# Kernel tuning notes

Measured on AMD Instinct MI355X. Metric: run time of the kernel, lower is better.

The kernel has to match this reference:

```python
import jax, jax.numpy as jnp
import numpy as np

LEAK = 0.2

def leaky(x):
    return jnp.where(x > 0, x, LEAK * x)

def relu(x):
    return jnp.maximum(x, 0)

def conv1d(x, w):
    # x [B,Cin,L], w [Cout,Cin,3], stride 1, padding 1
    return jax.lax.conv_general_dilated(x, w, (1,), [(1, 1)],
        dimension_numbers=('NCH', 'OIH', 'NCH'))

def conv2d(x, w, pad, dil=1, groups=1):
    return jax.lax.conv_general_dilated(x, w, (1, 1), [(pad, pad), (pad, pad)],
        rhs_dilation=(dil, dil), feature_group_count=groups,
        dimension_numbers=('NCHW', 'OIHW', 'NCHW'))

def bn2d(x, p, eps=1e-5):
    # p: [4,C] = gamma, beta, running_mean, running_var (eval-mode BN)
    g, b, m, v = p
    s = (1, -1, 1, 1)
    return (x - m.reshape(s)) * (g.reshape(s) / jnp.sqrt(v.reshape(s) + eps)) + b.reshape(s)

def layernorm(x, g, b, eps=1e-5):
    mu = x.mean(-1, keepdims=True)
    var = ((x - mu) ** 2).mean(-1, keepdims=True)
    return (x - mu) / jnp.sqrt(var + eps) * g + b

def l2n(x, axis, eps):
    n = jnp.sqrt((x * x).sum(axis, keepdims=True))
    return x / jnp.maximum(n, eps)


def setup_inputs() -> dict:
    key = jax.random.key(0)
    B, C, H, W = 4, 64, 48, 48
    D, Fn, T, V = 256, 8, 4, 16
    E = 16  # orthogonal prototype embed dim
    ks = iter(jax.random.split(key, 64))
    def rn(shape, s=0.05):
        return jax.random.normal(next(ks), shape, jnp.float32) * s
    def bnp(c):
        return jnp.stack([1.0 + rn((c,), 0.1), rn((c,), 0.1), rn((c,), 0.1), 1.0 + jnp.abs(rn((c,), 0.1))])
    return dict(
        basis_vector_bank=jax.random.normal(next(ks), (T, V, D), jnp.float32),
        task_f=jax.random.normal(next(ks), (B, C, 16, 16), jnp.float32),
        img_f=jax.random.normal(next(ks), (B, C, H, W), jnp.float32),
        protos=jax.random.normal(next(ks), (T, E), jnp.float32),
        tA_w1=rn((E // 4, 1, 3)), tA_w2=rn((E // 2, E // 4, 3)),
        iA_w=rn((E // 2, C, 3, 3)), iA_bn=bnp(E // 2),
        at_w1=rn((E, Fn // 2 * E)), at_b1=rn((Fn // 2 * E,)),
        at_ln_g=jnp.ones((Fn // 2 * E,)), at_ln_b=jnp.zeros((Fn // 2 * E,)),
        at_w2=rn((Fn // 2 * E, Fn * E)), at_b2=rn((Fn * E,)),
        bv_t1=rn((D // 4, 1, 3)), bv_t2=rn((D // 2, D // 4, 3)),
        bv_ic1=rn((D // 4, C, 3, 3)), bv_bn1=bnp(D // 4),
        bv_ic2=rn((D // 2, D // 4, 3, 3)), bv_bn2=bnp(D // 2),
        bv_w1=rn((D, D // 4)), bv_b1=rn((D // 4,)),
        bv_ln_g=jnp.ones((D // 4,)), bv_ln_b=jnp.zeros((D // 4,)),
        bv_w2=rn((D // 4, D)), bv_b2=rn((D,)),
        m1_w1=rn((D, D // 4)), m1_b1=rn((D // 4,)),
        m1_ln_g=jnp.ones((D // 4,)), m1_ln_b=jnp.zeros((D // 4,)),
        m1_w2=rn((D // 4, C * C)), m1_b2=rn((C * C,)),
        m3_w1=rn((D, D // 4)), m3_b1=rn((D // 4,)),
        m3_ln_g=jnp.ones((D // 4,)), m3_ln_b=jnp.zeros((D // 4,)),
        m3_w2=rn((D // 4, 9 * C * C)), m3_b2=rn((9 * C * C,)),
        blr_bn=bnp(C),
        zc_w=rn((C, C, 1, 1), 0.01), zc_b=rn((C,), 0.01),
    )


def _forward(basis_vector_bank, task_f, img_f, protos, tA_w1, tA_w2, iA_w, iA_bn,
             at_w1, at_b1, at_ln_g, at_ln_b, at_w2, at_b2,
             bv_t1, bv_t2, bv_ic1, bv_bn1, bv_ic2, bv_bn2,
             bv_w1, bv_b1, bv_ln_g, bv_ln_b, bv_w2, bv_b2,
             m1_w1, m1_b1, m1_ln_g, m1_ln_b, m1_w2, m1_b2,
             m3_w1, m3_b1, m3_ln_g, m3_ln_b, m3_w2, m3_b2,
             blr_bn, zc_w, zc_b):
    T, V, D = basis_vector_bank.shape
    B, C, H, W = img_f.shape
    E = protos.shape[1]
    Fn = at_w2.shape[1] // E
    tau = 0.5

    # --- A2SI routing features ---
    xt = task_f.reshape(B, 1, -1)
    t1 = conv1d(leaky(conv1d(xt, tA_w1)), tA_w2).mean(-1)          # [B,E/2]
    i1 = leaky(bn2d(conv2d(img_f, iA_w, 1), iA_bn)).mean((2, 3))   # [B,E/2]
    f1 = jnp.concatenate([t1, i1], axis=1)                         # [B,E]
    h = relu(layernorm(f1 @ at_w1 + at_b1, at_ln_g, at_ln_b))
    tif = (h @ at_w2 + at_b2).reshape(B, E, Fn)                    # [B,E,F]
    logits = jnp.einsum('te,bef->bft', l2n(protos, -1, 1e-8), l2n(tif, 1, 1e-8))  # [B,F,T]

    # hard gumbel-softmax (straight-through), fixed noise key for determinism
    u = jax.random.uniform(jax.random.key(42), logits.shape, jnp.float32, 1e-10, 1.0)
    g = -jnp.log(-jnp.log(u))
    y = jax.nn.softmax((logits + g) / tau, axis=-1)
    idx = jnp.argmax(y, axis=-1)                                   # [B,F]
    y_hard = jax.nn.one_hot(idx, T, dtype=y.dtype)
    set_type = y_hard + y - jax.lax.stop_gradient(y)

    bank_flat = basis_vector_bank.reshape(T, V * D)
    sbvb = jnp.einsum('bft,tk->bfk', set_type, bank_flat).reshape(B, Fn, V, D)

    # --- BasisV_filter: filter feature ---
    xt2 = task_f.reshape(B, C, -1)
    rms = jnp.sqrt((xt2 ** 2).mean((1, 2), keepdims=True))
    xt2 = (xt2 / (rms + 1e-8)).reshape(B, 1, -1)
    te = conv1d(leaky(conv1d(xt2, bv_t1)), bv_t2).mean(-1)         # [B,D/2]
    ie = leaky(bn2d(conv2d(img_f, bv_ic1, 1), bv_bn1))
    ie = leaky(bn2d(conv2d(ie, bv_ic2, 1), bv_bn2)).mean((2, 3))   # [B,D/2]
    ff = jnp.concatenate([te, ie], axis=1)                         # [B,D]
    ff = relu(layernorm(ff @ bv_w1 + bv_b1, bv_ln_g, bv_ln_b)) @ bv_w2 + bv_b2

    # --- per-(batch,type) group gather/top-k/scatter, vectorized ---
    # group bank = bank of first filter with that type (hard one-hot -> type's bank)
    occ = idx[:, None, :] == jnp.arange(T)[None, :, None]          # [B,T,F]
    first = jnp.argmax(occ, axis=-1)                               # [B,T]
    Bg = jnp.take_along_axis(sbvb, first[:, :, None, None], axis=1)  # [B,T,V,D]
    # all rows of Q within a group are identical (filter_f expanded over F),
    # so S.max(0) == cosine(ff[b], Bg[b,t])
    scores = jnp.einsum('bd,btvd->btv', l2n(ff, -1, 1e-12), l2n(Bg, -1, 1e-12))
    order = jnp.argsort(-scores, axis=-1)                          # [B,T,V] topk order
    lt = jnp.tril(jnp.ones((Fn, Fn), bool), -1)                    # j < i
    rank = ((idx[:, :, None] == idx[:, None, :]) & lt).sum(-1)     # position in group
    bidx = jnp.arange(B)[:, None]
    sel = order[bidx, idx, rank]                                   # [B,F]
    bvf = Bg[bidx, idx, sel]                                       # [B,F,D]

    # --- per-filter dynamic convolutions ---
    w1 = relu(layernorm(bvf @ m1_w1 + m1_b1, m1_ln_g, m1_ln_b)) @ m1_w2 + m1_b2
    w1 = w1.reshape(B, Fn, C, C)                                   # [B,F,out,in]
    w3 = relu(layernorm(bvf @ m3_w1 + m3_b1, m3_ln_g, m3_ln_b)) @ m3_w2 + m3_b2
    w3 = w3.reshape(B * Fn, C, C, 3, 3)

    dp0 = jnp.einsum('bfoc,bchw->bfohw', w1, img_f)                # 1x1 branch
    xin = jnp.broadcast_to(img_f[:, None], (B, Fn, C, H, W)).reshape(1, B * Fn * C, H, W)
    ker = w3.reshape(B * Fn * C, C, 3, 3)
    dpd = [conv2d(xin, ker, d, dil=d, groups=B * Fn).reshape(B, Fn, C, H, W)
           for d in (1, 2, 3)]                                     # same-padded dilated 3x3
    t_ = idx[:, :, None, None, None]
    dp = jnp.where(t_ == 0, dp0, jnp.where(t_ == 1, dpd[0],
         jnp.where(t_ == 2, dpd[1], dpd[2])))                      # [B,F,C,H,W]

    x = leaky(bn2d(dp.reshape(B * Fn, C, H, W), blr_bn)).reshape(B, Fn, C, H, W).mean(1)
    a = conv2d(x, zc_w, 0) + zc_b.reshape(1, -1, 1, 1)
    return a + img_f


@jax.jit
def reference(basis_vector_bank, task_f, img_f, protos, tA_w1, tA_w2, iA_w, iA_bn,
              at_w1, at_b1, at_ln_g, at_ln_b, at_w2, at_b2,
              bv_t1, bv_t2, bv_ic1, bv_bn1, bv_ic2, bv_bn2,
              bv_w1, bv_b1, bv_ln_g, bv_ln_b, bv_w2, bv_b2,
              m1_w1, m1_b1, m1_ln_g, m1_ln_b, m1_w2, m1_b2,
              m3_w1, m3_b1, m3_ln_g, m3_ln_b, m3_w2, m3_b2,
              blr_bn, zc_w, zc_b):
    return _forward(basis_vector_bank, task_f, img_f, protos, tA_w1, tA_w2, iA_w, iA_bn,
                    at_w1, at_b1, at_ln_g, at_ln_b, at_w2, at_b2,
                    bv_t1, bv_t2, bv_ic1, bv_bn1, bv_ic2, bv_bn2,
                    bv_w1, bv_b1, bv_ln_g, bv_ln_b, bv_w2, bv_b2,
                    m1_w1, m1_b1, m1_ln_g, m1_ln_b, m1_w2, m1_b2,
                    m3_w1, m3_b1, m3_ln_g, m3_ln_b, m3_w2, m3_b2,
                    blr_bn, zc_w, zc_b)
```

## Files before the change

### kernel.cpp

```cpp
#include <hip/hip_runtime.h>
#include <math.h>

#define LEAKC 0.2f

#define NB 4
#define NC 64
#define LLEN 16384
#define HW 2304
#define PP 54
#define PHW 2916
#define SLABP 72
#define CP 72
#define IE1C 50

typedef __attribute__((ext_vector_type(8))) short short8;
typedef __attribute__((ext_vector_type(4))) float floatx4;

__device__ __forceinline__ float leaky(float x){ return x > 0.f ? x : LEAKC*x; }

__device__ __forceinline__ float wave_sum64(float v){
  for(int off=32;off;off>>=1) v += __shfl_xor(v,off);
  return v;
}

__device__ __forceinline__ unsigned short f2bf(float x){
  unsigned u=__float_as_uint(x);
  unsigned r=u+0x7FFFu+((u>>16)&1u);
  return (unsigned short)(r>>16);
}

__device__ __forceinline__ void threefry2x32(unsigned k0, unsigned k1, unsigned& x0, unsigned& x1){
  unsigned ks0=k0, ks1=k1, ks2=k0^k1^0x1BD11BDAu;
  x0+=ks0; x1+=ks1;
  const int rot0[4]={13,15,26,6};
  const int rot1[4]={17,29,16,24};
#define TF_APPLY(rr) {for(int r=0;r<4;r++){x0+=x1; x1=(x1<<rr[r])|(x1>>(32-rr[r])); x1^=x0;}}
  TF_APPLY(rot0); x0+=ks1; x1+=ks2+1u;
  TF_APPLY(rot1); x0+=ks2; x1+=ks0+2u;
  TF_APPLY(rot0); x0+=ks0; x1+=ks1+3u;
  TF_APPLY(rot1); x0+=ks1; x1+=ks2+4u;
  TF_APPLY(rot0); x0+=ks2; x1+=ks0+5u;
#undef TF_APPLY
}

__device__ __forceinline__ float jax_uniform128(int i){
  unsigned x0=0u, x1=(unsigned)i;
  threefry2x32(0u,42u,x0,x1);
  unsigned bits = x0 ^ x1;
  unsigned fb=(bits>>9)|0x3f800000u;
  float f=__uint_as_float(fb)-1.0f;
  float u=f*(1.0f-1e-10f)+1e-10f;
  return fmaxf(1e-10f,u);
}

__global__ __launch_bounds__(256) void k_pre(const float* __restrict__ task_f,
                      const float* __restrict__ w1A, const float* __restrict__ w1B,
                      float* __restrict__ totApart, float* __restrict__ a0A, float* __restrict__ aLA,
                      float* __restrict__ totBpart, float* __restrict__ a0B, float* __restrict__ aLB,
                      float* __restrict__ rmspart,
                      const float* __restrict__ img,
                      const float* __restrict__ w1, const float* __restrict__ w2,
                      const float* __restrict__ wa,
                      unsigned short* __restrict__ imgTP,
                      unsigned short* __restrict__ W1T, unsigned short* __restrict__ W2T,
                      unsigned short* __restrict__ WAT,
                      const float* __restrict__ mw1, const float* __restrict__ mw3,
                      const float* __restrict__ bvw1p, const float* __restrict__ bvw2p,
                      const float* __restrict__ bvt2p, const float* __restrict__ atw2p,
                      const float* __restrict__ bankp, float* __restrict__ warm){
  if(blockIdx.x<256){
    int b=blockIdx.x>>6, seg=blockIdx.x&63;
    const float* x=task_f+b*LLEN;
    float tA[4]={0,0,0,0};
    float tB[64];
#pragma unroll
    for(int c=0;c<64;c++) tB[c]=0.f;
    float sq=0.f;
    int l=seg*256+threadIdx.x;
    {
      float xm=(l>0)?x[l-1]:0.f;
      float xc=x[l];
      float xp=(l<LLEN-1)?x[l+1]:0.f;
      sq=xc*xc;
#pragma unroll
      for(int c=0;c<4;c++){
        float a=leaky(w1A[c*3+0]*xm + w1A[c*3+1]*xc + w1A[c*3+2]*xp);
        tA[c]=a;
        if(l==0) a0A[b*4+c]=a;
        if(l==LLEN-1) aLA[b*4+c]=a;
      }
#pragma unroll
      for(int c=0;c<64;c++){
        float a=leaky(w1B[c*3+0]*xm + w1B[c*3+1]*xc + w1B[c*3+2]*xp);
        tB[c]=a;
        if(l==0) a0B[b*64+c]=a;
        if(l==LLEN-1) aLB[b*64+c]=a;
      }
    }
    sq=wave_sum64(sq);
#pragma unroll
    for(int c=0;c<4;c++) tA[c]=wave_sum64(tA[c]);
#pragma unroll
    for(int c=0;c<64;c++){
      float v=tB[c];
      for(int off=32;off;off>>=1) v+=__shfl_down(v,off);
      tB[c]=v;
    }
    __shared__ float redB[4][64];
    __shared__ float redA[4][4];
    __shared__ float redQ[4];
    int wave=threadIdx.x>>6, lane=threadIdx.x&63;
    if(lane==0){
#pragma unroll
      for(int c=0;c<64;c++) redB[wave][c]=tB[c];
#pragma unroll
      for(int c=0;c<4;c++) redA[wave][c]=tA[c];
      redQ[wave]=sq;
    }
    __syncthreads();
    if(threadIdx.x<64){
      float s=redB[0][threadIdx.x]+redB[1][threadIdx.x]+redB[2][threadIdx.x]+redB[3][threadIdx.x];
      totBpart[(size_t)(b*64+seg)*64+threadIdx.x]=s;
    } else if(threadIdx.x<68){
      int c=threadIdx.x-64;
      totApart[(b*64+seg)*4+c]=redA[0][c]+redA[1][c]+redA[2][c]+redA[3][c];
    } else if(threadIdx.x==68){
      rmspart[b*64+seg]=redQ[0]+redQ[1]+redQ[2]+redQ[3];
    }
  } else if(blockIdx.x<400){
    int blk=blockIdx.x-256;
    int b=blk/36, t=blk%36;
    int p0=t*64;
    __shared__ float tile[64][65];
    int pp=threadIdx.x&63, c4=threadIdx.x>>6;
    for(int r=0;r<16;r++){
      int c=c4*16+r;
      tile[c][pp]=img[(b*64+c)*HW + p0+pp];
    }
    __syncthreads();
    int pxl=threadIdx.x>>2, cg=(threadIdx.x&3)*16;
    unsigned out[8];
#pragma unroll
    for(int q=0;q<8;q++){
      unsigned lo=f2bf(tile[cg+2*q][pxl]);
      unsigned hi=f2bf(tile[cg+2*q+1][pxl]);
      out[q]=lo|(hi<<16);
    }
    int px=p0+pxl;
    int h=px/48, w=px-h*48;
    int poff=(h+3)*PP+(w+3);
    unsigned* dst=(unsigned*)(imgTP + ((size_t)(b*PHW+poff))*64 + cg);
#pragma unroll
    for(int q=0;q<8;q++) dst[q]=out[q];
  } else if(blockIdx.x<868){
    int n=(blockIdx.x-400)*256+threadIdx.x;
    if(n<9*64*64){
      int tap=n>>12, oc=(n>>6)&63, c=n&63;
      W1T[n]=f2bf(w1[oc*576+c*9+tap]);
    } else if(n<9*64*64+9*128*64){
      int m=n-9*64*64;
      int tap=m/8192, r=m-tap*8192, oc=r>>6, c=r&63;
      W2T[m]=f2bf(w2[oc*576+c*9+tap]);
    } else {
      int q=n-9*64*64-9*128*64;
      if(q<9*16*64){
        int tap=q>>10, r=q&1023, o=r>>6, c=r&63;
        WAT[q]=(o<8)?f2bf(wa[o*576+c*9+tap]):(unsigned short)0;
      }
    }
  } else if(blockIdx.x<884){
    int t=(blockIdx.x-868)*256+threadIdx.x;
    float a=0.f;
    for(int i=t;i*16<16384;i+=4096) a+=mw1[i*16];
    for(int i=t;i*16<16384;i+=4096) a+=mw3[i*16];
    for(int i=t;i*16<16384;i+=4096) a+=bvw1p[i*16];
    for(int i=t;i*16<16384;i+=4096) a+=bvw2p[i*16];
    for(int i=t;i*16<24576;i+=4096) a+=bvt2p[i*16];
    for(int i=t;i*16<8192;i+=4096) a+=atw2p[i*16];
    for(int i=t;i*16<16384;i+=4096) a+=bankp[i*16];
    warm[t&1023]=a;
  } else {
    int id=(blockIdx.x-884)*256+threadIdx.x;
    uint4 z=make_uint4(0,0,0,0);
    for(int cch=id;cch<19584;cch+=4096){
      int ck=cch&7, pxid=cch>>3;
      int b=pxid/612, p=pxid-b*612;
      int h,w;
      if(p<324){ int r=p/54; w=p-r*54; h=(r<3)?r:(r+48); }
      else { int q=p-324; int r2=q/6; int cc=q-r2*6; h=3+r2; w=(cc<3)?cc:(cc+48); }
      *(uint4*)(imgTP + ((size_t)(b*PHW + h*PP + w))*64 + ck*8)=z;
    }
  }
}

__global__ __launch_bounds__(512) void k_conv12(const unsigned short* __restrict__ imgTP,
                        const unsigned short* __restrict__ W1T,
                        const unsigned short* __restrict__ W2T,
                        const unsigned short* __restrict__ WAT,
                        const float* __restrict__ bn1, const float* __restrict__ bn2,
                        const float* __restrict__ bnA,
                        float* __restrict__ iepart, float* __restrict__ i1part){
  int tid=threadIdx.x;
  int lane=tid&63, wv=tid>>6;
  int n0=lane&15, kg=lane>>4;
  if(blockIdx.x<96){
    int blk=blockIdx.x;
    int b=blk/24, hp=blk-b*24;
    int h0=hp*2;
    __shared__ unsigned short slab[6*54*SLABP];
    __shared__ unsigned short ie1[4*IE1C*CP];
    {
      const unsigned short* ibase=imgTP+((size_t)b*PHW+(size_t)(h0+1)*PP)*64;
      for(int e=tid;e<6*54*8;e+=512){
        int rr=e/(54*8), rem=e-rr*54*8, w=rem>>3, ck=rem&7;
        uint4 v=*(const uint4*)(ibase+((size_t)(rr*PP+w))*64+ck*8);
        *(uint4*)(slab+(rr*54+w)*SLABP+ck*8)=v;
      }
      if(tid<64){
        int br=tid>>4, cq=(tid>>3)&1, ck=tid&7;
        *(uint4*)(ie1+((size_t)(br*IE1C+(cq?49:0)))*CP+ck*8)=make_uint4(0,0,0,0);
      }
    }
    __syncthreads();
    {
      int mt=wv&3, rh=wv>>2;
      floatx4 acc[2][3];
#pragma unroll
      for(int rr=0;rr<2;rr++)
#pragma unroll
        for(int nt=0;nt<3;nt++) acc[rr][nt]=(floatx4){0.f,0.f,0.f,0.f};
#pragma unroll
      for(int ti=0;ti<3;ti++){
#pragma unroll
        for(int tj=0;tj<3;tj++){
          int tap=ti*3+tj;
          const unsigned short* Ab=W1T+(size_t)tap*4096;
#pragma unroll
          for(int c0=0;c0<64;c0+=32){
            short8 a=*(const short8*)(Ab+((mt*16+n0)*64+c0+kg*8));
#pragma unroll
            for(int rr=0;rr<2;rr++){
              int sr=rh*2+rr+ti;
#pragma unroll
              for(int nt=0;nt<3;nt++){
                int sc=nt*16+n0+tj+2;
                short8 bv=*(const short8*)(slab+(sr*54+sc)*SLABP+c0+kg*8);
                acc[rr][nt]=__builtin_amdgcn_mfma_f32_16x16x32_bf16(a,bv,acc[rr][nt],0,0,0);
              }
            }
          }
        }
      }
      int obase=mt*16+kg*4;
      float scale[4],m_[4],be_[4];
#pragma unroll
      for(int reg=0;reg<4;reg++){
        int o=obase+reg;
        scale[reg]=bn1[o]/sqrtf(bn1[192+o]+1e-5f);
        m_[reg]=bn1[128+o]; be_[reg]=bn1[64+o];
      }
#pragma unroll
      for(int rr=0;rr<2;rr++){
        int br=rh*2+rr;
        bool rv=((unsigned)(h0-1+br))<48u;
#pragma unroll
        for(int nt=0;nt<3;nt++){
          float v0=rv?leaky((acc[rr][nt][0]-m_[0])*scale[0]+be_[0]):0.f;
          float v1=rv?leaky((acc[rr][nt][1]-m_[1])*scale[1]+be_[1]):0.f;
          float v2=rv?leaky((acc[rr][nt][2]-m_[2])*scale[2]+be_[2]):0.f;
          float v3=rv?leaky((acc[rr][nt][3]-m_[3])*scale[3]+be_[3]):0.f;
          unsigned w0=f2bf(v0)|((unsigned)f2bf(v1)<<16);
          unsigned w1=f2bf(v2)|((unsigned)f2bf(v3)<<16);
          uint2 pk={w0,w1};
          *(uint2*)(ie1+((size_t)(br*IE1C+(nt*16+1+n0)))*CP+obase)=pk;
        }
      }
    }
    __syncthreads();
    {
      int mt2=wv;
      floatx4 acc[6];
#pragma unroll
      for(int i=0;i<6;i++) acc[i]=(floatx4){0.f,0.f,0.f,0.f};
#pragma unroll
      for(int ti=0;ti<3;ti++){
#pragma unroll
        for(int tj=0;tj<3;tj++){
          int tap=ti*3+tj;
          const unsigned short* Ab=W2T+(size_t)tap*8192;
#pragma unroll
          for(int c0=0;c0<64;c0+=32){
            short8 a=*(const short8*)(Ab+((mt2*16+n0)*64+c0+kg*8));
#pragma unroll
            for(int rr=0;rr<2;rr++){
              int sr=rr+ti;
#pragma unroll
              for(int wc=0;wc<3;wc++){
                int q=wc*16+n0+tj;
                short8 bv=*(const short8*)(ie1+((size_t)(sr*IE1C+q))*CP+c0+kg*8);
                acc[rr*3+wc]=__builtin_amdgcn_mfma_f32_16x16x32_bf16(a,bv,acc[rr*3+wc],0,0,0);
              }
            }
          }
        }
      }
      int obase=mt2*16+kg*4;
#pragma unroll
      for(int reg=0;reg<4;reg++){
        int o=obase+reg;
        float scale=bn2[o]/sqrtf(bn2[384+o]+1e-5f);
        float m_=bn2[256+o], be_=bn2[128+o];
        float part=0;
#pragma unroll
        for(int i=0;i<6;i++) part+=leaky((acc[i][reg]-m_)*scale+be_);
        for(int off=1;off<16;off<<=1) part+=__shfl_xor(part,off);
        if(n0==0) iepart[(b*24+hp)*128+o]=part*(1.f/2304.f);
      }
    }
  } else {
    int blk2=blockIdx.x-96;
    int b=blk2/3, hg=blk2-b*3;
    int hp=hg*8+wv;
    int h0=hp*2;
    const unsigned short* ib=imgTP+(size_t)b*PHW*64;
    floatx4 acc[6];
#pragma unroll
    for(int i=0;i<6;i++) acc[i]=(floatx4){0.f,0.f,0.f,0.f};
#pragma unroll
    for(int ti=0;ti<3;ti++){
#pragma unroll
      for(int tj=0;tj<3;tj++){
        int tap=ti*3+tj;
        const unsigned short* Ab=WAT+(size_t)tap*1024;
#pragma unroll
        for(int c0=0;c0<64;c0+=32){
          short8 a=*(const short8*)(Ab+(n0*64+c0+kg*8));
#pragma unroll
          for(int rr=0;rr<2;rr++){
            int r=h0+rr+ti-1+3;
#pragma unroll
            for(int wc=0;wc<3;wc++){
              int w=wc*16+n0+tj-1+3;
              short8 bv=*(const short8*)(ib+((size_t)(r*PP+w)*64+c0+kg*8));
              acc[rr*3+wc]=__builtin_amdgcn_mfma_f32_16x16x32_bf16(a,bv,acc[rr*3+wc],0,0,0);
            }
          }
        }
      }
    }
    int obase=kg*4;
#pragma unroll
    for(int reg=0;reg<4;reg++){
      int o=obase+reg;
      float part=0;
      if(o<8){
        float scale=bnA[o]/sqrtf(bnA[24+o]+1e-5f);
        float m_=bnA[16+o], be_=bnA[8+o];
#pragma unroll
        for(int i=0;i<6;i++) part+=leaky((acc[i][reg]-m_)*scale+be_);
      }
      for(int off=1;off<16;off<<=1) part+=__shfl_xor(part,off);
      if(n0==0 && o<8) i1part[(b*24+hp)*8+o]=part*(1.f/2304.f);
    }
  }
}

__global__ __launch_bounds__(512,1) void k_mid(
    const float* __restrict__ totApart, const float* __restrict__ a0A, const float* __restrict__ aLA,
    const float* __restrict__ totBpart, const float* __restrict__ a0B, const float* __restrict__ aLB,
    const float* __restrict__ rmspart,
    const float* __restrict__ tA_w2, const float* __restrict__ bv_t2,
    const float* __restrict__ i1part, const float* __restrict__ iepart,
    const float* __restrict__ at_w1, const float* __restrict__ at_b1,
    const float* __restrict__ at_ln_g, const float* __restrict__ at_ln_b,
    const float* __restrict__ at_w2, const float* __restrict__ at_b2,
    const float* __restrict__ protos,
    const float* __restrict__ bv_w1, const float* __restrict__ bv_b1,
    const float* __restrict__ bv_ln_g, const float* __restrict__ bv_ln_b,
    const float* __restrict__ bv_w2, const float* __restrict__ bv_b2,
    const float* __restrict__ bank,
    const float* __restrict__ m1_w1, const float* __restrict__ m1_b1,
    const float* __restrict__ m1_g,  const float* __restrict__ m1_bb,
    const float* __restrict__ m3_w1, const float* __restrict__ m3_b1,
    const float* __restrict__ m3_g,  const float* __restrict__ m3_bb,
    int* __restrict__ idxo, float* __restrict__ hid1, float* __restrict__ hid3){
  int b=blockIdx.x;
  int tid=threadIdx.x;
  int lane=tid&63, wv=tid>>6;
  const float invL=1.0f/16384.0f;
  __shared__ float sT[64], s0[64], sL[64];
  __shared__ float totA_s[4];
  __shared__ float rms_s;
  __shared__ float part[512];
  __shared__ float te_s[128], t1_s[8];
  __shared__ float f1[16], h[64], tif[128], tifn[128], tden[8], pden[4], pn[64], z[32];
  __shared__ int sidx[8], sfirst[4], srank[8], rows[8];
  __shared__ float fbuf[256], hh[64], ffn_s[256], finv_s;
  __shared__ float scores[64];
  __shared__ int order[64];
  __shared__ float bvf[2048];

  if(tid<64){
    float s=0;
#pragma unroll 8
    for(int seg=0;seg<64;seg++) s+=totBpart[(size_t)(b*64+seg)*64+tid];
    sT[tid]=s;
  } else if(tid<128){
    int t=tid-64;
    s0[t]=a0B[b*64+t]; sL[t]=aLB[b*64+t];
  } else if(tid<192){
    float v=rmspart[b*64+(tid-128)];
    v=wave_sum64(v);
    if(tid==128) rms_s=v;
  } else if(tid<256){
    int c=tid-192;
    if(c<4){
      float s=0;
#pragma unroll 8
      for(int seg=0;seg<64;seg++) s+=totApart[(b*64+seg)*4+c];
      totA_s[c]=s;
    }
  }
  __syncthreads();
  float scB=1.0f/(sqrtf(rms_s*invL)+1e-8f);
  if(tid<256){
    int c2=tid&127, h2=tid>>7;
    const float* wr=bv_t2+c2*192;
    float s=0;
    for(int c1=h2*32;c1<h2*32+32;c1+=8){
      float4 q[6];
      const float4* r4=(const float4*)(wr+c1*3);
#pragma unroll
      for(int u=0;u<6;u++) q[u]=r4[u];
      const float* qq=(const float*)q;
#pragma unroll
      for(int u=0;u<8;u++){
        int c=c1+u;
        float T=sT[c], A0=s0[c], AL=sL[c];
        s += qq[u*3+0]*(T-AL) + qq[u*3+1]*T + qq[u*3+2]*(T-A0);
      }
    }
    part[tid]=s;
  } else if(tid>=384 && tid<392){
    int c2=tid-384;
    float s=0;
    for(int c1=0;c1<4;c1++){
      float T=totA_s[c1], A0=a0A[b*4+c1], AL=aLA[b*4+c1];
      const float* w=&tA_w2[(c2*4+c1)*3];
      s += w[0]*(T-AL) + w[1]*T + w[2]*(T-A0);
    }
    t1_s[c2]=s*invL;
  }
  __syncthreads();
  if(tid<128) te_s[tid]=(part[tid]+part[tid+128])*invL*scB;
  __syncthreads();

  if(tid<8) f1[tid]=t1_s[tid];
  else if(tid<16){
    int f=tid-8;
    float s=0;
#pragma unroll
    for(int g=0;g<24;g++) s+=i1part[(b*24+g)*8+f];
    f1[tid]=s;
  }
  __syncthreads();
  if(tid<64){
    float s=at_b1[lane];
#pragma unroll
    for(int i=0;i<16;i++) s+=f1[i]*at_w1[i*64+lane];
    float mu=wave_sum64(s)*(1.f/64.f);
    float d=s-mu;
    float var=wave_sum64(d*d)*(1.f/64.f);
    h[lane]=fmaxf(d*(1.0f/sqrtf(var+1e-5f))*at_ln_g[lane]+at_ln_b[lane],0.f);
  }
  __syncthreads();
  if(tid<256){
    int n=tid&127, h2=tid>>7;
    float a0=0,a1=0;
    for(int k=h2*32;k<h2*32+32;k+=2){
      a0+=h[k]*at_w2[k*128+n];
      a1+=h[k+1]*at_w2[(k+1)*128+n];
    }
    part[tid]=a0+a1;
  }
  __syncthreads();
  if(tid<128) tif[tid]=at_b2[tid]+part[tid]+part[tid+128];
  __syncthreads();
  if(tid<8){
    int f=tid;
    float ss=0; for(int e=0;e<16;e++){float v=tif[e*8+f]; ss+=v*v;}
    tden[f]=fmaxf(sqrtf(ss),1e-8f);
  } else if(tid<12){
    int t=tid-8;
    float ss=0; for(int e=0;e<16;e++){float v=protos[t*16+e]; ss+=v*v;}
    pden[t]=fmaxf(sqrtf(ss),1e-8f);
  }
  __syncthreads();
  if(tid<128) tifn[tid]=tif[tid]/tden[tid&7];
  if(tid<64) pn[tid]=protos[tid]/pden[tid>>4];
  __syncthreads();
  if(tid<32){
    int f=tid>>2, t=tid&3;
    float ss=0;
#pragma unroll
    for(int e=0;e<16;e++) ss+=pn[t*16+e]*tifn[e*8+f];
    float u=jax_uniform128(b*32+f*4+t);
    float g=-logf(-logf(u));
    z[tid]=ss+g;
  }
  __syncthreads();
  if(tid<8){
    float best=z[tid*4]; int bi=0;
    for(int t=1;t<4;t++){ float v=z[tid*4+t]; if(v>best){best=v;bi=t;} }
    sidx[tid]=bi;
  }
  __syncthreads();
  if(tid<4){
    int t=tid;
    int fi=0;
    for(int f=7;f>=0;f--) if(sidx[f]==t) fi=f;
    sfirst[t]=fi;
  } else if(tid<12){
    int f=tid-4;
    int c=0; for(int f2=0;f2<f;f2++) if(sidx[f2]==sidx[f]) c++;
    srank[f]=c;
  }
  __syncthreads();

  if(tid<128) fbuf[tid]=te_s[tid];
  else if(tid<256){
    int c=tid-128;
    float s=0;
#pragma unroll 8
    for(int g=0;g<24;g++) s+=iepart[(b*24+g)*128+c];
    fbuf[tid]=s;
  }
  __syncthreads();
  if(tid<256){
    int l64=tid&63, q=tid>>6;
    float a0=0,a1=0,a2=0,a3=0;
    for(int k=q*64;k<q*64+64;k+=4){
      a0+=fbuf[k]  *bv_w1[k*64+l64];
      a1+=fbuf[k+1]*bv_w1[(k+1)*64+l64];
      a2+=fbuf[k+2]*bv_w1[(k+2)*64+l64];
      a3+=fbuf[k+3]*bv_w1[(k+3)*64+l64];
    }
    part[tid]=((a0+a1)+(a2+a3));
  }
  __syncthreads();
  if(tid<64){
    float s=bv_b1[lane]+part[lane]+part[64+lane]+part[128+lane]+part[192+lane];
    float mu=wave_sum64(s)*(1.f/64.f);
    float d=s-mu;
    float var=wave_sum64(d*d)*(1.f/64.f);
    hh[lane]=fmaxf(d*(1.0f/sqrtf(var+1e-5f))*bv_ln_g[lane]+bv_ln_b[lane],0.f);
  }
  __syncthreads();
  {
    int n=tid&255, h2=tid>>8;
    float a0=0,a1=0;
    for(int k=h2*32;k<h2*32+32;k+=2){
      a0+=hh[k]*bv_w2[k*256+n];
      a1+=hh[k+1]*bv_w2[(k+1)*256+n];
    }
    part[tid]=a0+a1;
  }
  __syncthreads();
  if(tid<256) ffn_s[tid]=bv_b2[tid]+part[tid]+part[tid+256];
  __syncthreads();
  if(tid<64){
    float sq=0;
#pragma unroll
    for(int u=0;u<4;u++){ float v=ffn_s[u*64+lane]; sq+=v*v; }
    sq=wave_sum64(sq);
    if(lane==0) finv_s=1.0f/fmaxf(sqrtf(sq),1e-12f);
  }
  __syncthreads();
  if(tid<256) ffn_s[tid]*=finv_s;
  __syncthreads();

  if(tid<128){
    int it=tid&63, h2=tid>>6;
    int t=it>>4, v=it&15;
    int tt=sidx[sfirst[t]];
    const float4* row=(const float4*)(bank+(tt*16+v)*256);
    float sa=0,na=0;
    for(int d4=h2*32;d4<h2*32+32;d4++){
      float4 r=row[d4];
      const float* fp=&ffn_s[d4*4];
      sa+=fp[0]*r.x+fp[1]*r.y+fp[2]*r.z+fp[3]*r.w;
      na+=r.x*r.x+r.y*r.y+r.z*r.z+r.w*r.w;
    }
    part[tid]=sa;
    part[256+tid]=na;
  }
  __syncthreads();
  if(tid<64) scores[tid]=(part[tid]+part[tid+64])/fmaxf(sqrtf(part[256+tid]+part[320+tid]),1e-12f);
  __syncthreads();
  if(tid<4){
    const float* sc=&scores[tid*16];
    unsigned used=0;
    for(int pk=0;pk<16;pk++){
      int best=-1; float bv=-1e30f;
      for(int v2=0;v2<16;v2++){
        if(used&(1u<<v2)) continue;
        float vv=sc[v2];
        if(best<0||vv>bv){bv=vv;best=v2;}
      }
      used|=1u<<best;
      order[tid*16+pk]=best;
    }
  }
  __syncthreads();
  if(tid<8){
    int t=sidx[tid];
    int v=order[t*16+srank[tid]];
    rows[tid]=t*16+v;
    idxo[b*8+tid]=t;
  }
  __syncthreads();

  for(int ii=tid;ii<2048;ii+=512){
    int r=ii>>8, d=ii&255;
    bvf[ii]=bank[rows[r]*256+d];
  }
  __syncthreads();
  {
    int r=wv;
    const float* bp=&bvf[r*256];
    float a0=0,a1=0,a2=0,a3=0;
    float c0=0,c1=0,c2=0,c3=0;
    for(int d=0;d<256;d+=4){
      float b0=bp[d],b1=bp[d+1],b2=bp[d+2],b3=bp[d+3];
      a0+=b0*m1_w1[d*64+lane];
      a1+=b1*m1_w1[(d+1)*64+lane];
      a2+=b2*m1_w1[(d+2)*64+lane];
      a3+=b3*m1_w1[(d+3)*64+lane];
      c0+=b0*m3_w1[d*64+lane];
      c1+=b1*m3_w1[(d+1)*64+lane];
      c2+=b2*m3_w1[(d+2)*64+lane];
      c3+=b3*m3_w1[(d+3)*64+lane];
    }
    float s1=m1_b1[lane]+((a0+a1)+(a2+a3));
    float s3=m3_b1[lane]+((c0+c1)+(c2+c3));
    float mu=wave_sum64(s1)*(1.f/64.f);
    float dd=s1-mu;
    float var=wave_sum64(dd*dd)*(1.f/64.f);
    hid1[(b*8+r)*64+lane]=fmaxf(dd*(1.0f/sqrtf(var+1e-5f))*m1_g[lane]+m1_bb[lane],0.f);
    mu=wave_sum64(s3)*(1.f/64.f);
    dd=s3-mu;
    var=wave_sum64(dd*dd)*(1.f/64.f);
    hid3[(b*8+r)*64+lane]=fmaxf(dd*(1.0f/sqrtf(var+1e-5f))*m3_g[lane]+m3_bb[lane],0.f);
  }
}

__global__ __launch_bounds__(256) void k_heads(const float* __restrict__ hid1, const float* __restrict__ hid3,
                        const float* __restrict__ w2a, const float* __restrict__ b2a,
                        const float* __restrict__ w2b, const float* __restrict__ b2b,
                        unsigned short* __restrict__ A1, unsigned short* __restrict__ A3){
  __shared__ float hl[2048];
  if(blockIdx.x<16){
    int n=blockIdx.x*256+threadIdx.x;
    for(int i=threadIdx.x;i<2048;i+=256) hl[i]=hid1[i];
    __syncthreads();
    float wcol[64];
#pragma unroll
    for(int k=0;k<64;k++) wcol[k]=w2a[k*4096+n];
    float bb=b2a[n];
    for(int bf=0;bf<32;bf++){
      float s=bb;
#pragma unroll
      for(int k=0;k<64;k++) s+=hl[bf*64+k]*wcol[k];
      A1[bf*4096+n]=f2bf(s);
    }
  } else {
    int n=(blockIdx.x-16)*256+threadIdx.x;
    for(int i=threadIdx.x;i<2048;i+=256) hl[i]=hid3[i];
    __syncthreads();
    float wcol[64];
#pragma unroll
    for(int k=0;k<64;k++) wcol[k]=w2b[(size_t)k*36864+n];
    float bb=b2b[n];
    int o=n/576, rem=n-o*576;
    int c=rem/9, tap=rem-c*9;
    size_t base=((size_t)tap*64+o)*64+c;
    for(int bf=0;bf<32;bf++){
      float s=bb;
#pragma unroll
      for(int k=0;k<64;k++) s+=hl[bf*64+k]*wcol[k];
      A3[(size_t)bf*9*4096+base]=f2bf(s);
    }
  }
}

__global__ __launch_bounds__(512) void k_dynF(const unsigned short* __restrict__ imgTP,
                       const unsigned short* __restrict__ A1, const unsigned short* __restrict__ A3,
                       const int* __restrict__ idx, const float* __restrict__ bn,
                       const float* __restrict__ zc_w, const float* __restrict__ zc_b,
                       const float* __restrict__ img, float* __restrict__ out){
  int blk=blockIdx.x;
  int b=blk/48, r0=blk-b*48;
  int tid=threadIdx.x;
  int lane=tid&63, w8=tid>>6;
  int mt=w8&3, fh=w8>>2;
  int n0=lane&15, kg=lane>>4;
  __shared__ unsigned short slab[7*54*SLABP];
  __shared__ float xl[64*50];
  __shared__ float zl[4096];
  for(int i=tid;i<4096;i+=512) zl[i]=zc_w[i];
  for(int i=tid;i<3200;i+=512) xl[i]=0.f;
  {
    const unsigned short* ibase=imgTP+((size_t)b*PHW+(size_t)r0*PP)*64;
    for(int e=tid;e<7*54*8;e+=512){
      int rr=e/(54*8), rem=e-rr*54*8, w=rem>>3, ck=rem&7;
      uint4 v=*(const uint4*)(ibase + ((size_t)(rr*PP+w))*64 + ck*8);
      *(uint4*)(slab + (rr*54+w)*SLABP + ck*8)=v;
    }
  }
  __syncthreads();
  int obase=mt*16+kg*4;
  float scale[4],m_[4],be_[4];
#pragma unroll
  for(int reg=0;reg<4;reg++){
    int o=obase+reg;
    scale[reg]=bn[o]/sqrtf(bn[192+o]+1e-5f);
    m_[reg]=bn[128+o]; be_[reg]=bn[64+o];
  }
  float xsum[3][4];
#pragma unroll
  for(int wc=0;wc<3;wc++)
#pragma unroll
    for(int reg=0;reg<4;reg++) xsum[wc][reg]=0.f;
  for(int f=fh*4;f<fh*4+4;f++){
    int bf=b*8+f;
    int tt=idx[bf];
    floatx4 acc[3];
#pragma unroll
    for(int i=0;i<3;i++) acc[i]=(floatx4){0.f,0.f,0.f,0.f};
    if(tt==0){
      const unsigned short* Ab=A1+(size_t)bf*4096;
#pragma unroll
      for(int c0=0;c0<64;c0+=32){
        short8 a=*(const short8*)(Ab+((mt*16+n0)*64+c0+kg*8));
#pragma unroll
        for(int wc=0;wc<3;wc++){
          short8 bv=*(const short8*)(slab + (3*54 + wc*16+n0+3)*SLABP + c0+kg*8);
          acc[wc]=__builtin_amdgcn_mfma_f32_16x16x32_bf16(a,bv,acc[wc],0,0,0);
        }
      }
    } else {
      int d=tt;
      const unsigned short* A3b=A3+(size_t)bf*9*4096;
#pragma unroll
      for(int ti=0;ti<3;ti++){
        int lr=d*(ti-1)+3;
#pragma unroll
        for(int tj=0;tj<3;tj++){
          int tap=ti*3+tj;
          int dw=d*(tj-1)+3;
          const unsigned short* Ab=A3b+(size_t)tap*4096;
#pragma unroll
          for(int c0=0;c0<64;c0+=32){
            short8 a=*(const short8*)(Ab+((mt*16+n0)*64+c0+kg*8));
#pragma unroll
            for(int wc=0;wc<3;wc++){
              short8 bv=*(const short8*)(slab + (lr*54 + wc*16+n0+dw)*SLABP + c0+kg*8);
              acc[wc]=__builtin_amdgcn_mfma_f32_16x16x32_bf16(a,bv,acc[wc],0,0,0);
            }
          }
        }
      }
    }
#pragma unroll
    for(int wc=0;wc<3;wc++)
#pragma unroll
      for(int reg=0;reg<4;reg++)
        xsum[wc][reg]+=leaky((acc[wc][reg]-m_[reg])*scale[reg]+be_[reg]);
  }
#pragma unroll
  for(int wc=0;wc<3;wc++)
#pragma unroll
    for(int reg=0;reg<4;reg++)
      atomicAdd(&xl[(obase+reg)*50 + wc*16+n0], xsum[wc][reg]*0.125f);
  __syncthreads();
  size_t base=(size_t)b*64*HW + r0*48;
  for(int e=tid;e<3072;e+=512){
    int o=e/48, px=e-o*48;
    float s=zc_b[o];
#pragma unroll
    for(int c=0;c<64;c++) s+=zl[o*64+c]*xl[c*50+px];
    size_t a=base+(size_t)o*HW+px;
    out[a]=s+img[a];
  }
}

extern "C" void kernel_launch(void* const* d_in, const int* in_sizes, int n_in,
                              void* d_out, int out_size, void* d_ws, size_t ws_size,
                              hipStream_t stream){
  const float* bank   =(const float*)d_in[0];
  const float* task_f =(const float*)d_in[1];
  const float* img_f  =(const float*)d_in[2];
  const float* protos =(const float*)d_in[3];
  const float* tA_w1  =(const float*)d_in[4];
  const float* tA_w2  =(const float*)d_in[5];
  const float* iA_w   =(const float*)d_in[6];
  const float* iA_bn  =(const float*)d_in[7];
  const float* at_w1  =(const float*)d_in[8];
  const float* at_b1  =(const float*)d_in[9];
  const float* at_ln_g=(const float*)d_in[10];
  const float* at_ln_b=(const float*)d_in[11];
  const float* at_w2  =(const float*)d_in[12];
  const float* at_b2  =(const float*)d_in[13];
  const float* bv_t1  =(const float*)d_in[14];
  const float* bv_t2  =(const float*)d_in[15];
  const float* bv_ic1 =(const float*)d_in[16];
  const float* bv_bn1 =(const float*)d_in[17];
  const float* bv_ic2 =(const float*)d_in[18];
  const float* bv_bn2 =(const float*)d_in[19];
  const float* bv_w1  =(const float*)d_in[20];
  const float* bv_b1  =(const float*)d_in[21];
  const float* bv_ln_g=(const float*)d_in[22];
  const float* bv_ln_b=(const float*)d_in[23];
  const float* bv_w2  =(const float*)d_in[24];
  const float* bv_b2  =(const float*)d_in[25];
  const float* m1_w1  =(const float*)d_in[26];
  const float* m1_b1  =(const float*)d_in[27];
  const float* m1_ln_g=(const float*)d_in[28];
  const float* m1_ln_b=(const float*)d_in[29];
  const float* m1_w2  =(const float*)d_in[30];
  const float* m1_b2  =(const float*)d_in[31];
  const float* m3_w1  =(const float*)d_in[32];
  const float* m3_b1  =(const float*)d_in[33];
  const float* m3_ln_g=(const float*)d_in[34];
  const float* m3_ln_b=(const float*)d_in[35];
  const float* m3_w2  =(const float*)d_in[36];
  const float* m3_b2  =(const float*)d_in[37];
  const float* blr_bn =(const float*)d_in[38];
  const float* zc_w   =(const float*)d_in[39];
  const float* zc_b   =(const float*)d_in[40];

  float* ws=(float*)d_ws;
  float* totApart=ws+0;
  float* a0A  =ws+1024;
  float* aLA  =ws+1040;
  float* totBpart=ws+1056;
  float* a0B  =ws+17440;
  float* aLB  =ws+17696;
  float* rmspart=ws+17952;
  float* i1part =ws+18208;
  float* iepart =ws+18976;
  int*   idxp   =(int*)(ws+31264);
  float* hid1=ws+31296;
  float* hid3=ws+33344;
  unsigned short* A1p  =(unsigned short*)(ws+35392);
  unsigned short* A3p  =(unsigned short*)(ws+100928);
  unsigned short* imgTP=(unsigned short*)(ws+690752);
  unsigned short* W1Tp =(unsigned short*)(ws+1064000);
  unsigned short* W2Tp =(unsigned short*)(ws+1082432);
  unsigned short* WATp =(unsigned short*)(ws+1119296);
  float* warm =ws+1123904;

  k_pre<<<900,256,0,stream>>>(task_f, tA_w1, bv_t1,
                              totApart, a0A, aLA, totBpart, a0B, aLB, rmspart,
                              img_f, bv_ic1, bv_ic2, iA_w, imgTP, W1Tp, W2Tp, WATp,
                              m1_w1, m3_w1, bv_w1, bv_w2, bv_t2, at_w2, bank, warm);
  k_conv12<<<108,512,0,stream>>>(imgTP, W1Tp, W2Tp, WATp, bv_bn1, bv_bn2, iA_bn,
                                 iepart, i1part);
  k_mid<<<4,512,0,stream>>>(totApart,a0A,aLA,totBpart,a0B,aLB, rmspart, tA_w2, bv_t2,
                            i1part, iepart,
                            at_w1, at_b1, at_ln_g, at_ln_b, at_w2, at_b2, protos,
                            bv_w1, bv_b1, bv_ln_g, bv_ln_b, bv_w2, bv_b2, bank,
                            m1_w1, m1_b1, m1_ln_g, m1_ln_b,
                            m3_w1, m3_b1, m3_ln_g, m3_ln_b,
                            idxp, hid1, hid3);
  k_heads<<<160,256,0,stream>>>(hid1, hid3, m1_w2, m1_b2, m3_w2, m3_b2, A1p, A3p);
  k_dynF<<<192,512,0,stream>>>(imgTP, A1p, A3p, idxp, blr_bn, zc_w, zc_b, img_f, (float*)d_out);

  (void)in_sizes; (void)n_in; (void)out_size; (void)ws_size;
}
```

Baseline: 267.2 us.

## Expand cache prefetch warmup, parallelize k_mid reduction, hoist loads above barriers

The k_pre warm-up blocks grow from 16 to 64 and now also touch the large head weights (m1_w2, m3_w2) and zc_w at one line per 64 bytes, to pull them into L2 ahead of k_heads and k_dynF. k_mid spreads the totBpart reduction over all 512 threads with a shared-memory second stage, and its idle threads prefetch the weights it reads later. k_heads and k_dynF issue weight, idx and BN-parameter loads before the shared-memory fill and barrier so that latency overlaps. The cost is more global traffic and blocks in k_pre, plus an extra barrier in k_mid.

```diff
diff --git a/kernel.cpp b/kernel.cpp
--- a/kernel.cpp
+++ b/kernel.cpp
@@ -67,7 +67,10 @@
                       const float* __restrict__ mw1, const float* __restrict__ mw3,
                       const float* __restrict__ bvw1p, const float* __restrict__ bvw2p,
                       const float* __restrict__ bvt2p, const float* __restrict__ atw2p,
-                      const float* __restrict__ bankp, float* __restrict__ warm){
+                      const float* __restrict__ bankp,
+                      const float* __restrict__ m1w2p, const float* __restrict__ m3w2p,
+                      const float* __restrict__ zcwp,
+                      float* __restrict__ warm){
   if(blockIdx.x<256){
     int b=blockIdx.x>>6, seg=blockIdx.x&63;
     const float* x=task_f+b*LLEN;
@@ -168,19 +171,22 @@
         WAT[q]=(o<8)?f2bf(wa[o*576+c*9+tap]):(unsigned short)0;
       }
     }
-  } else if(blockIdx.x<884){
+  } else if(blockIdx.x<932){
     int t=(blockIdx.x-868)*256+threadIdx.x;
     float a=0.f;
-    for(int i=t;i*16<16384;i+=4096) a+=mw1[i*16];
-    for(int i=t;i*16<16384;i+=4096) a+=mw3[i*16];
-    for(int i=t;i*16<16384;i+=4096) a+=bvw1p[i*16];
-    for(int i=t;i*16<16384;i+=4096) a+=bvw2p[i*16];
-    for(int i=t;i*16<24576;i+=4096) a+=bvt2p[i*16];
-    for(int i=t;i*16<8192;i+=4096) a+=atw2p[i*16];
-    for(int i=t;i*16<16384;i+=4096) a+=bankp[i*16];
+    for(int i=t;i*16<16384;i+=16384) a+=mw1[i*16];
+    for(int i=t;i*16<16384;i+=16384) a+=mw3[i*16];
+    for(int i=t;i*16<16384;i+=16384) a+=bvw1p[i*16];
+    for(int i=t;i*16<16384;i+=16384) a+=bvw2p[i*16];
+    for(int i=t;i*16<24576;i+=16384) a+=bvt2p[i*16];
+    for(int i=t;i*16<8192;i+=16384) a+=atw2p[i*16];
+    for(int i=t;i*16<16384;i+=16384) a+=bankp[i*16];
+    for(int i=t;i*16<262144;i+=16384) a+=m1w2p[i*16];
+    for(int i=t;i*16<2359296;i+=16384) a+=m3w2p[i*16];
+    for(int i=t;i*16<4096;i+=16384) a+=zcwp[i*16];
     warm[t&1023]=a;
   } else {
-    int id=(blockIdx.x-884)*256+threadIdx.x;
+    int id=(blockIdx.x-932)*256+threadIdx.x;
     uint4 z=make_uint4(0,0,0,0);
     for(int cch=id;cch<19584;cch+=4096){
       int ck=cch&7, pxid=cch>>3;
@@ -389,6 +395,7 @@
   int lane=tid&63, wv=tid>>6;
   const float invL=1.0f/16384.0f;
   __shared__ float sT[64], s0[64], sL[64];
+  __shared__ float red8[64][9];
   __shared__ float totA_s[4];
   __shared__ float rms_s;
   __shared__ float part[512];
@@ -400,26 +407,46 @@
   __shared__ int order[64];
   __shared__ float bvf[2048];
 
-  if(tid<64){
-    float s=0;
-#pragma unroll 8
-    for(int seg=0;seg<64;seg++) s+=totBpart[(size_t)(b*64+seg)*64+tid];
-    sT[tid]=s;
-  } else if(tid<128){
+  {
+    int c8=tid>>3, g8=tid&7;
+    float s8=0;
+#pragma unroll
+    for(int seg=g8*8;seg<g8*8+8;seg++) s8+=totBpart[(size_t)(b*64+seg)*64+c8];
+    red8[c8][g8]=s8;
+  }
+  if(tid>=64 && tid<128){
     int t=tid-64;
     s0[t]=a0B[b*64+t]; sL[t]=aLB[b*64+t];
-  } else if(tid<192){
+  } else if(tid>=128 && tid<192){
     float v=rmspart[b*64+(tid-128)];
     v=wave_sum64(v);
     if(tid==128) rms_s=v;
-  } else if(tid<256){
+  } else if(tid>=192 && tid<196){
     int c=tid-192;
-    if(c<4){
-      float s=0;
+    float s=0;
 #pragma unroll 8
-      for(int seg=0;seg<64;seg++) s+=totApart[(b*64+seg)*4+c];
-      totA_s[c]=s;
-    }
+    for(int seg=0;seg<64;seg++) s+=totApart[(b*64+seg)*4+c];
+    totA_s[c]=s;
+  } else if(tid>=256){
+    int t=tid-256;
+    float ax=0.f,ay=0.f,az=0.f,aw=0.f;
+    const float4* p;
+    p=(const float4*)bv_t2;  for(int i=t;i<6144;i+=256){float4 v=p[i]; ax+=v.x;ay+=v.y;az+=v.z;aw+=v.w;}
+    p=(const float4*)at_w2;  for(int i=t;i<2048;i+=256){float4 v=p[i]; ax+=v.x;ay+=v.y;az+=v.z;aw+=v.w;}
+    p=(const float4*)bv_w1;  for(int i=t;i<4096;i+=256){float4 v=p[i]; ax+=v.x;ay+=v.y;az+=v.z;aw+=v.w;}
+    p=(const float4*)bv_w2;  for(int i=t;i<4096;i+=256){float4 v=p[i]; ax+=v.x;ay+=v.y;az+=v.z;aw+=v.w;}
+    p=(const float4*)m1_w1;  for(int i=t;i<4096;i+=256){float4 v=p[i]; ax+=v.x;ay+=v.y;az+=v.z;aw+=v.w;}
+    p=(const float4*)m3_w1;  for(int i=t;i<4096;i+=256){float4 v=p[i]; ax+=v.x;ay+=v.y;az+=v.z;aw+=v.w;}
+    p=(const float4*)bank;   for(int i=t;i<4096;i+=256){float4 v=p[i]; ax+=v.x;ay+=v.y;az+=v.z;aw+=v.w;}
+    float s=ax+ay+az+aw;
+    asm volatile("" :: "v"(s));
+  }
+  __syncthreads();
+  if(tid<64){
+    float s=0;
+#pragma unroll
+    for(int g=0;g<8;g++) s+=red8[tid][g];
+    sT[tid]=s;
   }
   __syncthreads();
   float scB=1.0f/(sqrtf(rms_s*invL)+1e-8f);
@@ -661,12 +688,12 @@
   __shared__ float hl[2048];
   if(blockIdx.x<16){
     int n=blockIdx.x*256+threadIdx.x;
+    float wcol[64];
+#pragma unroll
+    for(int k=0;k<64;k++) wcol[k]=w2a[k*4096+n];
+    float bb=b2a[n];
     for(int i=threadIdx.x;i<2048;i+=256) hl[i]=hid1[i];
     __syncthreads();
-    float wcol[64];
-#pragma unroll
-    for(int k=0;k<64;k++) wcol[k]=w2a[k*4096+n];
-    float bb=b2a[n];
     for(int bf=0;bf<32;bf++){
       float s=bb;
 #pragma unroll
@@ -675,12 +702,12 @@
     }
   } else {
     int n=(blockIdx.x-16)*256+threadIdx.x;
+    float wcol[64];
+#pragma unroll
+    for(int k=0;k<64;k++) wcol[k]=w2b[(size_t)k*36864+n];
+    float bb=b2b[n];
     for(int i=threadIdx.x;i<2048;i+=256) hl[i]=hid3[i];
     __syncthreads();
-    float wcol[64];
-#pragma unroll
-    for(int k=0;k<64;k++) wcol[k]=w2b[(size_t)k*36864+n];
-    float bb=b2b[n];
     int o=n/576, rem=n-o*576;
     int c=rem/9, tap=rem-c*9;
     size_t base=((size_t)tap*64+o)*64+c;
@@ -707,6 +734,17 @@
   __shared__ unsigned short slab[7*54*SLABP];
   __shared__ float xl[64*50];
   __shared__ float zl[4096];
+  int tts[4];
+#pragma unroll
+  for(int i=0;i<4;i++) tts[i]=idx[b*8+fh*4+i];
+  int obase=mt*16+kg*4;
+  float scale[4],m_[4],be_[4];
+#pragma unroll
+  for(int reg=0;reg<4;reg++){
+    int o=obase+reg;
+    scale[reg]=bn[o]/sqrtf(bn[192+o]+1e-5f);
+    m_[reg]=bn[128+o]; be_[reg]=bn[64+o];
+  }
   for(int i=tid;i<4096;i+=512) zl[i]=zc_w[i];
   for(int i=tid;i<3200;i+=512) xl[i]=0.f;
   {
@@ -718,22 +756,16 @@
     }
   }
   __syncthreads();
-  int obase=mt*16+kg*4;
-  float scale[4],m_[4],be_[4];
-#pragma unroll
-  for(int reg=0;reg<4;reg++){
-    int o=obase+reg;
-    scale[reg]=bn[o]/sqrtf(bn[192+o]+1e-5f);
-    m_[reg]=bn[128+o]; be_[reg]=bn[64+o];
-  }
   float xsum[3][4];
 #pragma unroll
   for(int wc=0;wc<3;wc++)
 #pragma unroll
     for(int reg=0;reg<4;reg++) xsum[wc][reg]=0.f;
-  for(int f=fh*4;f<fh*4+4;f++){
+#pragma unroll
+  for(int fi=0;fi<4;fi++){
+    int f=fh*4+fi;
     int bf=b*8+f;
-    int tt=idx[bf];
+    int tt=tts[fi];
     floatx4 acc[3];
 #pragma unroll
     for(int i=0;i<3;i++) acc[i]=(floatx4){0.f,0.f,0.f,0.f};
@@ -860,10 +892,11 @@
   unsigned short* WATp =(unsigned short*)(ws+1119296);
   float* warm =ws+1123904;
 
-  k_pre<<<900,256,0,stream>>>(task_f, tA_w1, bv_t1,
+  k_pre<<<948,256,0,stream>>>(task_f, tA_w1, bv_t1,
                               totApart, a0A, aLA, totBpart, a0B, aLB, rmspart,
                               img_f, bv_ic1, bv_ic2, iA_w, imgTP, W1Tp, W2Tp, WATp,
-                              m1_w1, m3_w1, bv_w1, bv_w2, bv_t2, at_w2, bank, warm);
+                              m1_w1, m3_w1, bv_w1, bv_w2, bv_t2, at_w2, bank,
+                              m1_w2, m3_w2, zc_w, warm);
   k_conv12<<<108,512,0,stream>>>(imgTP, W1Tp, W2Tp, WATp, bv_bn1, bv_bn2, iA_bn,
                                  iepart, i1part);
   k_mid<<<4,512,0,stream>>>(totApart,a0A,aLA,totBpart,a0B,aLB, rmspart, tA_w2, bv_t2,
```

New measurement: 294.5 us. +10.2%, slower.
